# Kernel tuning notes

Measured on AMD Instinct MI355X. Metric: run time of the kernel, lower is better.

## Reference

```python
import jax, jax.numpy as jnp
import numpy as np

# dims (see shape_source)
B, NC, DIM_IN = 4, 4095, 64      # batch, cells, invariant state dim (n-6)
D, H, L, K = 128, 4, 2, 6        # d_model, heads, layers, num_neighbors
DH = D // H                      # dim_head = 32
HR, NRBF = 16, 16                # radial hidden dim (d_model//8), rbf basis
RBF_MAX, RBF_W = 4.0, 0.25


def _ln(x, s, b):
    m = x.mean(-1, keepdims=True)
    v = x.var(-1, keepdims=True)
    return (x - m) / jnp.sqrt(v + 1e-5) * s + b


def setup_inputs() -> dict:
    key = jax.random.key(0)
    ks = jax.random.split(key, 32)
    def nrm(k, shape, scale):
        return jax.random.normal(k, shape, jnp.float32) * scale
    p = {}
    p['X'] = nrm(ks[0], (B, NC, 6 + DIM_IN), 1.0)
    p['W_embed'] = nrm(ks[1], (DIM_IN, D), DIM_IN ** -0.5)
    p['b_embed'] = jnp.zeros((D,), jnp.float32)
    p['Wq'] = nrm(ks[2], (L, D, D), D ** -0.5)
    p['Wk'] = nrm(ks[3], (L, D, D), D ** -0.5)
    p['Wv'] = nrm(ks[4], (L, D, D), D ** -0.5)
    p['Wvv'] = nrm(ks[5], (L, D, D), D ** -0.5)
    p['rw1'] = nrm(ks[6], (L, NRBF, HR), NRBF ** -0.5)
    p['rb1'] = jnp.zeros((L, HR), jnp.float32)
    p['rw2'] = nrm(ks[7], (L, HR, 2 * D), HR ** -0.5)
    p['rb2'] = jnp.zeros((L, 2 * D), jnp.float32)
    p['Wo'] = nrm(ks[8], (L, D, D), D ** -0.5)
    p['Wov'] = nrm(ks[9], (L, D, D), D ** -0.5)
    p['ff_w1'] = nrm(ks[10], (L, D, 2 * D), D ** -0.5)
    p['ff_b1'] = jnp.zeros((L, 2 * D), jnp.float32)
    p['ff_w2'] = nrm(ks[11], (L, 2 * D, D), (2 * D) ** -0.5)
    p['ff_b2'] = jnp.zeros((L, D), jnp.float32)
    p['gate_w'] = nrm(ks[12], (L, D, D), D ** -0.5)
    p['gate_b'] = jnp.zeros((L, D), jnp.float32)
    p['ln1_s'] = jnp.ones((L, D), jnp.float32)
    p['ln1_b'] = jnp.zeros((L, D), jnp.float32)
    p['ln2_s'] = jnp.ones((L, D), jnp.float32)
    p['ln2_b'] = jnp.zeros((L, D), jnp.float32)
    p['W_state'] = nrm(ks[13], (D, DIM_IN), D ** -0.5)
    p['b_state'] = jnp.zeros((DIM_IN,), jnp.float32)
    p['W_force'] = nrm(ks[14], (D, 1), D ** -0.5)
    p['b_force'] = jnp.zeros((1,), jnp.float32)
    return p


def _forward(X, W_embed, b_embed, Wq, Wk, Wv, Wvv, rw1, rb1, rw2, rb2, Wo, Wov,
             ff_w1, ff_b1, ff_w2, ff_b2, gate_w, gate_b,
             ln1_s, ln1_b, ln2_s, ln2_b, W_state, b_state, W_force, b_force):
    N = NC + 1  # one extra zero node prepended, as in the torch wrapper
    pos = jnp.concatenate([jnp.zeros((B, 1, 3), X.dtype), X[:, :, 0:3]], axis=1)       # [B,N,3]
    feats = jnp.concatenate([jnp.zeros((B, 1, DIM_IN), X.dtype), X[:, :, 6:]], axis=1)  # [B,N,dim_in]

    # k-nearest-neighbor graph (indices are non-differentiable constants)
    d2 = jnp.sum((pos[:, :, None, :] - pos[:, None, :, :]) ** 2, axis=-1)  # [B,N,N]
    d2 = d2 + jnp.eye(N, dtype=X.dtype) * 1e9                               # exclude self
    _, idx = jax.lax.top_k(-d2, K)                                           # [B,N,K]

    gat = lambda a: jax.vmap(lambda ai, ii: ai[ii])(a, idx)  # [B,N,...] -> [B,N,K,...]

    rel = gat(pos) - pos[:, :, None, :]                      # [B,N,K,3]
    dist = jnp.sqrt(jnp.sum(rel ** 2, axis=-1) + 1e-8)       # [B,N,K]
    u = rel / dist[..., None]                                # unit vectors (degree-1 SH)
    centers = jnp.linspace(0.0, RBF_MAX, NRBF).astype(X.dtype)
    rbf = jnp.exp(-((dist[..., None] - centers) / RBF_W) ** 2)  # [B,N,K,NRBF]

    x0 = feats @ W_embed + b_embed                           # type-0 (invariant) feats
    x1 = jnp.zeros((B, N, D, 3), X.dtype)                    # type-1 (vector) feats

    for l in range(L):
        h = _ln(x0, ln1_s[l], ln1_b[l])
        q = (h @ Wq[l]).reshape(B, N, H, DH)
        kj = gat(h @ Wk[l]).reshape(B, N, K, H, DH)
        vj = gat(h @ Wv[l])                                   # [B,N,K,D]
        # radial MLP on distances -> invariant edge weights
        rad = jax.nn.silu(rbf @ rw1[l] + rb1[l]) @ rw2[l] + rb2[l]  # [B,N,K,2D]
        rg, rv = rad[..., :D], rad[..., D:]
        bias = rg.reshape(B, N, K, H, DH).mean(-1)            # [B,N,K,H]
        logits = jnp.einsum('bnhd,bnkhd->bnhk', q, kj) / np.float32(np.sqrt(DH))
        logits = logits + bias.transpose(0, 1, 3, 2)
        attn = jax.nn.softmax(logits, axis=-1)                # over K neighbors
        # degree-0 messages
        m0 = (vj * jax.nn.silu(rv)).reshape(B, N, K, H, DH)
        out0 = jnp.einsum('bnhk,bnkhd->bnhd', attn, m0).reshape(B, N, D)
        x0 = x0 + out0 @ Wo[l]
        # degree-1 messages: channel-mixed neighbor vectors + radial-weighted unit dirs
        x1j = gat(x1)                                          # [B,N,K,D,3]
        m1 = jnp.einsum('bnkdc,de->bnkec', x1j, Wvv[l]) + rv[..., None] * u[:, :, :, None, :]
        m1 = m1.reshape(B, N, K, H, DH, 3)
        out1 = jnp.einsum('bnhk,bnkhdc->bnhdc', attn, m1).reshape(B, N, D, 3)
        x1 = x1 + jnp.einsum('bndc,de->bnec', out1, Wov[l])
        # feed-forward on invariants + invariant gating of vectors (equivariant)
        h2 = _ln(x0, ln2_s[l], ln2_b[l])
        x0 = x0 + jax.nn.silu(h2 @ ff_w1[l] + ff_b1[l]) @ ff_w2[l] + ff_b2[l]
        x1 = x1 * jax.nn.sigmoid(h2 @ gate_w[l] + gate_b[l])[..., None]

    y0 = x0[:, 1:]                                            # drop extra node
    y1 = jnp.swapaxes(x1[:, 1:], -1, -2)                      # [B,NC,3,D]
    state_update = y0 @ W_state + b_state                     # [B,NC,dim_in]
    forces = (y1 @ W_force + b_force)[..., 0]                 # [B,NC,3]
    forces = forces - forces.mean(axis=1, keepdims=True)      # remove net force
    return state_update, forces


def reference(X, W_embed, b_embed, Wq, Wk, Wv, Wvv, rw1, rb1, rw2, rb2, Wo, Wov,
              ff_w1, ff_b1, ff_w2, ff_b2, gate_w, gate_b,
              ln1_s, ln1_b, ln2_s, ln2_b, W_state, b_state, W_force, b_force):
    return _forward(X, W_embed, b_embed, Wq, Wk, Wv, Wvv, rw1, rb1, rw2, rb2, Wo, Wov,
                    ff_w1, ff_b1, ff_w2, ff_b2, gate_w, gate_b,
                    ln1_s, ln1_b, ln2_s, ln2_b, W_state, b_state, W_force, b_force)
```

## Files before the change

### kernel.cpp

```cpp
#include <hip/hip_runtime.h>
#include <cstdint>
#include <cstddef>

namespace {

constexpr int B_ = 4, NC_ = 4095, N_ = 4096, DIN_ = 64, D_ = 128, K_ = 6;
constexpr int XROW_ = 6 + DIN_;
constexpr int ROWS_ = B_ * N_;
constexpr int KNQ = 2;
constexpr int KCAP = 32;

typedef unsigned short u16;
typedef unsigned int u32;
typedef unsigned long long u64;
typedef __attribute__((ext_vector_type(8))) short short8;
typedef __attribute__((ext_vector_type(8))) unsigned short ushort8;
typedef __attribute__((ext_vector_type(4))) float f32x4;

__device__ __forceinline__ float sigm(float x) { return 1.f / (1.f + expf(-x)); }
__device__ __forceinline__ float silu(float x) { return x / (1.f + expf(-x)); }
__device__ __forceinline__ u16 f2bf(float x) {
    u32 u = __float_as_uint(x);
    u += 0x7FFFu + ((u >> 16) & 1u);
    return (u16)(u >> 16);
}
__device__ __forceinline__ float bf2f(u16 x) {
    return __uint_as_float(((u32)x) << 16);
}

__global__ void k_prep(const float* __restrict__ X, float4* __restrict__ pos4,
                       u16* __restrict__ featsb)
{
    int g = blockIdx.x * 256 + threadIdx.x;
    if (g >= ROWS_ * 64) return;
    int c = g & 63, row = g >> 6;
    int b = row >> 12, n = row & (N_ - 1);
    const float* xr = X + (size_t)(b * NC_ + n - 1) * XROW_;
    featsb[g] = (n > 0) ? f2bf(xr[6 + c]) : (u16)0;
    if (c == 0) {
        float4 p = {0.f, 0.f, 0.f, 0.f};
        if (n > 0) { p.x = xr[0]; p.y = xr[1]; p.z = xr[2]; }
        pos4[row] = p;
    }
}

__device__ __forceinline__ u64 shflxor64(u64 v, int mask)
{
    int lo = __shfl_xor((int)(u32)(v & 0xffffffffull), mask, 64);
    int hi = __shfl_xor((int)(u32)(v >> 32), mask, 64);
    return ((u64)(u32)hi << 32) | (u32)lo;
}

__device__ __forceinline__ float kth6min(float v)
{
    const float BIG = 3.4e38f;
    float kth = BIG;
    #pragma unroll
    for (int r = 0; r < 6; ++r) {
        float m = v;
        #pragma unroll
        for (int off = 1; off < 64; off <<= 1) m = fminf(m, __shfl_xor(m, off, 64));
        kth = m;
        if (v == m) v = BIG;
    }
    return kth;
}

__device__ __forceinline__ void geom_write(const float4* __restrict__ pb, int q, int j,
                                           size_t e, float* __restrict__ uv,
                                           float* __restrict__ rbfv)
{
    float4 pj = pb[j], pn = pb[q];
    float rx = pj.x - pn.x, ry = pj.y - pn.y, rz = pj.z - pn.z;
    float dist = sqrtf(rx * rx + ry * ry + rz * rz + 1e-8f);
    float inv = 1.f / dist;
    uv[e * 3 + 0] = rx * inv; uv[e * 3 + 1] = ry * inv; uv[e * 3 + 2] = rz * inv;
    #pragma unroll
    for (int r = 0; r < 16; ++r) {
        float t = (dist - (4.0f / 15.0f) * r) * 4.0f;
        rbfv[e * 16 + r] = expf(-t * t);
    }
}

__global__ __launch_bounds__(256) void k_knn(const float4* __restrict__ pos4,
                                             int* __restrict__ idxv,
                                             float* __restrict__ uv,
                                             float* __restrict__ rbfv)
{
    __shared__ u64 sHits[4][KNQ][KCAP];
    __shared__ int sCnt[4][KNQ];
    const int w = threadIdx.x >> 6, lane = threadIdx.x & 63;
    const int wave = (blockIdx.x << 2) | w;
    const int b = wave >> 11;
    const int i0 = (wave & 2047) << 1;
    const float4* pb = pos4 + (size_t)b * N_;
    const float BIG = 3.4e38f;

    if (lane < KNQ) sCnt[w][lane] = 0;
    __syncthreads();

    float4 qv[KNQ];
    #pragma unroll
    for (int qq = 0; qq < KNQ; ++qq) qv[qq] = pb[i0 + qq];

    float dmin[KNQ];
    #pragma unroll
    for (int qq = 0; qq < KNQ; ++qq) dmin[qq] = BIG;
    #pragma unroll 4
    for (int it = 0; it < 64; ++it) {
        int j = lane + (it << 6);
        float4 p = pb[j];
        #pragma unroll
        for (int qq = 0; qq < KNQ; ++qq) {
            float dx = p.x - qv[qq].x, dy = p.y - qv[qq].y, dz = p.z - qv[qq].z;
            float dd = dx * dx + dy * dy + dz * dz;
            if (j != i0 + qq) dmin[qq] = fminf(dmin[qq], dd);
        }
    }
    float T[KNQ];
    #pragma unroll
    for (int qq = 0; qq < KNQ; ++qq) T[qq] = kth6min(dmin[qq]) * 1.000002f;

    #pragma unroll 4
    for (int it = 0; it < 64; ++it) {
        int j = lane + (it << 6);
        float4 p = pb[j];
        #pragma unroll
        for (int qq = 0; qq < KNQ; ++qq) {
            float dx = p.x - qv[qq].x, dy = p.y - qv[qq].y, dz = p.z - qv[qq].z;
            float dd = dx * dx + dy * dy + dz * dz;
            if (dd <= T[qq] && j != i0 + qq) {
                int slot = atomicAdd(&sCnt[w][qq], 1);
                if (slot < KCAP)
                    sHits[w][qq][slot] = ((u64)__float_as_uint(dd) << 32) | (u32)j;
            }
        }
    }
    __syncthreads();

    const int g = lane >> 5, li = lane & 31;
    const int cnt = sCnt[w][g];
    const int q = i0 + g;
    u64 ent = (li < (cnt < KCAP ? cnt : KCAP)) ? sHits[w][g][li] : ~0ull;
    int myj = -1;
    #pragma unroll
    for (int k = 0; k < 6; ++k) {
        u64 m = ent;
        #pragma unroll
        for (int off = 1; off < 32; off <<= 1) {
            u64 o = shflxor64(m, off);
            if (o < m) m = o;
        }
        if (li == k) myj = (int)(u32)(m & 0xffffffffull);
        if (ent == m) ent = ~0ull;
    }
    if (cnt <= KCAP && li < 6) {
        size_t e = (size_t)(b * N_ + q) * 6 + li;
        idxv[e] = myj;
        geom_write(pb, q, myj, e, uv, rbfv);
    }

    u64 ovf = __ballot(li == 0 && cnt > KCAP);
    while (ovf) {
        int gl = __ffsll(ovf) - 1; ovf &= ovf - 1;
        int qq = gl >> 5;
        int qx = i0 + qq;
        float4 qp = pb[qx];
        float Tq = T[0];
        #pragma unroll
        for (int z = 1; z < KNQ; ++z) if (z == qq) Tq = T[z];
        float e0 = BIG, e1 = BIG, e2 = BIG, e3 = BIG, e4 = BIG, e5 = BIG;
        int j0 = 0, j1 = 0, j2 = 0, j3 = 0, j4 = 0, j5 = 0;
        for (int it = 0; it < 64; ++it) {
            int j = lane + (it << 6);
            float4 p = pb[j];
            float dx = p.x - qp.x, dy = p.y - qp.y, dz = p.z - qp.z;
            float dd = dx * dx + dy * dy + dz * dz;
            if (dd <= Tq && j != qx && dd < e5) {
                e5 = dd; j5 = j;
                float td; int tj;
                if (e5 < e4) { td = e4; e4 = e5; e5 = td; tj = j4; j4 = j5; j5 = tj; }
                if (e4 < e3) { td = e3; e3 = e4; e4 = td; tj = j3; j3 = j4; j4 = tj; }
                if (e3 < e2) { td = e2; e2 = e3; e3 = td; tj = j2; j2 = j3; j3 = tj; }
                if (e2 < e1) { td = e1; e1 = e2; e2 = td; tj = j1; j1 = j2; j2 = tj; }
                if (e1 < e0) { td = e0; e0 = e1; e1 = td; tj = j0; j0 = j1; j1 = tj; }
            }
        }
        u64 a0 = ((u64)__float_as_uint(e0) << 32) | (u32)j0;
        u64 a1 = ((u64)__float_as_uint(e1) << 32) | (u32)j1;
        u64 a2 = ((u64)__float_as_uint(e2) << 32) | (u32)j2;
        u64 a3 = ((u64)__float_as_uint(e3) << 32) | (u32)j3;
        u64 a4 = ((u64)__float_as_uint(e4) << 32) | (u32)j4;
        u64 a5 = ((u64)__float_as_uint(e5) << 32) | (u32)j5;
        int fj = -1;
        #pragma unroll
        for (int k = 0; k < 6; ++k) {
            u64 m = a0;
            #pragma unroll
            for (int off = 1; off < 64; off <<= 1) {
                u64 o = shflxor64(m, off);
                if (o < m) m = o;
            }
            if (a0 == m) { a0 = a1; a1 = a2; a2 = a3; a3 = a4; a4 = a5; a5 = ~0ull; }
            if (lane == k) fj = (int)(u32)(m & 0xffffffffull);
        }
        if (lane < 6) {
            size_t e = (size_t)(b * N_ + qx) * 6 + lane;
            idxv[e] = fj;
            geom_write(pb, qx, fj, e, uv, rbfv);
        }
    }
}

__global__ void k_prepw(const float* __restrict__ Wq, const float* __restrict__ Wk,
                        const float* __restrict__ Wv, const float* __restrict__ gw,
                        const float* __restrict__ fw1, const float* __restrict__ gb_,
                        const float* __restrict__ fb1, const float* __restrict__ Wvv,
                        const float* __restrict__ Wov, const float* __restrict__ Wo_,
                        const float* __restrict__ fw2, const float* __restrict__ rw2,
                        const float* __restrict__ rb2, const float* __restrict__ W_embed,
                        const float* __restrict__ rw1,
                        u16* __restrict__ WqkvT, u16* __restrict__ Wc2T,
                        u16* __restrict__ WvvT, u16* __restrict__ WovT,
                        u16* __restrict__ WoT, u16* __restrict__ fw2T,
                        u16* __restrict__ WembT,
                        float* __restrict__ bias2, float* __restrict__ rwg,
                        float* __restrict__ rw1T, float* __restrict__ rw2vT)
{
    const int l = blockIdx.y;
    int g = blockIdx.x * 256 + threadIdx.x;
    const float* Wq_l = Wq + l * 16384;  const float* Wk_l = Wk + l * 16384;
    const float* Wv_l = Wv + l * 16384;  const float* gw_l = gw + l * 16384;
    const float* fw1_l = fw1 + l * 32768; const float* gb_l = gb_ + l * 128;
    const float* fb1_l = fb1 + l * 256;  const float* Wvv_l = Wvv + l * 16384;
    const float* Wov_l = Wov + l * 16384; const float* Wo_ll = Wo_ + l * 16384;
    const float* fw2_l = fw2 + l * 32768; const float* rw2_l = rw2 + l * 4096;
    const float* rb2_l = rb2 + l * 256;  const float* rw1_l = rw1 + l * 256;

    if (g < 49152) {
        int n = g >> 7, k = g & 127;
        const float* src = (n < 128) ? Wq_l : ((n < 256) ? Wk_l : Wv_l);
        WqkvT[l * 49152 + g] = f2bf(src[k * 128 + (n & 127)]); return;
    }
    g -= 49152;
    if (g < 49152) {
        int n = g >> 7, k = g & 127;
        Wc2T[l * 49152 + g] = f2bf((n < 128) ? gw_l[k * 128 + n] : fw1_l[k * 256 + (n - 128)]); return;
    }
    g -= 49152;
    if (g < 16384) { int n = g >> 7, k = g & 127; WvvT[l * 16384 + g] = f2bf(Wvv_l[k * 128 + n]); return; }
    g -= 16384;
    if (g < 16384) { int n = g >> 7, k = g & 127; WovT[l * 16384 + g] = f2bf(Wov_l[k * 128 + n]); return; }
    g -= 16384;
    if (g < 16384) { int n = g >> 7, k = g & 127; WoT[l * 16384 + g] = f2bf(Wo_ll[k * 128 + n]); return; }
    g -= 16384;
    if (g < 32768) { int n = g >> 8, k = g & 255; fw2T[l * 32768 + g] = f2bf(fw2_l[k * 128 + n]); return; }
    g -= 32768;
    if (g < 384) { bias2[l * 384 + g] = (g < 128) ? gb_l[g] : fb1_l[g - 128]; return; }
    g -= 384;
    if (g < 64) {
        int hh = g >> 2, h = g & 3;
        float a = 0.f;
        #pragma unroll
        for (int dh = 0; dh < 32; ++dh) a += rw2_l[hh * 256 + h * 32 + dh];
        rwg[l * 128 + g] = a * (1.f / 32.f); return;
    }
    g -= 64;
    if (g < 4) {
        float a = 0.f;
        #pragma unroll
        for (int dh = 0; dh < 32; ++dh) a += rb2_l[g * 32 + dh];
        rwg[l * 128 + 64 + g] = a * (1.f / 32.f); return;
    }
    g -= 4;
    if (g < 256) {
        int hh = g >> 4, rr = g & 15;
        rw1T[l * 256 + hh * 16 + rr] = rw1_l[rr * 16 + hh]; return;
    }
    g -= 256;
    if (g < 2048) {
        int t = g >> 4, hh = g & 15;
        rw2vT[l * 2048 + t * 16 + hh] = rw2_l[hh * 256 + 128 + t]; return;
    }
    g -= 2048;
    if (g < 8192 && l == 0) {
        int n = g >> 6, k = g & 63;
        WembT[g] = f2bf(W_embed[k * 128 + n]);
    }
}

template<int KD, int BM, int EPI, bool LN, bool X1ACC>
__global__ __launch_bounds__(256) void k_mgemm(
    const u16* __restrict__ A, const u16* __restrict__ WT,
    const float* __restrict__ bias, const float* __restrict__ aux,
    float* __restrict__ C, u16* __restrict__ Cb, int ldc,
    const float* __restrict__ lns, const float* __restrict__ lnb,
    u16* __restrict__ lnout)
{
    constexpr int MI = BM / 16;
    __shared__ u16 sA[BM * 40];
    __shared__ u16 sB[128 * 40];
    const int tid = threadIdx.x;
    const int lane = tid & 63, wn = tid >> 6;
    const int m0 = blockIdx.x * BM, n0 = blockIdx.y * 128;
    f32x4 acc[MI][2] = {};

    for (int k0 = 0; k0 < KD; k0 += 32) {
        __syncthreads();
        if (BM == 64) {
            int row = tid >> 2, gk = tid & 3;
            *(uint4*)&sA[row * 40 + gk * 8] =
                *(const uint4*)&A[(size_t)(m0 + row) * KD + k0 + gk * 8];
        } else {
            if (tid < BM * 4) {
                int row = tid >> 2, gk = tid & 3;
                *(uint4*)&sA[row * 40 + gk * 8] =
                    *(const uint4*)&A[(size_t)(m0 + row) * KD + k0 + gk * 8];
            }
        }
        #pragma unroll
        for (int cc = 0; cc < 2; ++cc) {
            int c = tid * 2 + cc;
            int row = c >> 2, gk = c & 3;
            *(uint4*)&sB[row * 40 + gk * 8] =
                *(const uint4*)&WT[(size_t)(n0 + row) * KD + k0 + gk * 8];
        }
        __syncthreads();
        const int gk = lane >> 4, lr = lane & 15;
        short8 af[MI], bfr[2];
        #pragma unroll
        for (int i = 0; i < MI; ++i)
            af[i] = *(const short8*)&sA[(i * 16 + lr) * 40 + gk * 8];
        #pragma unroll
        for (int i = 0; i < 2; ++i)
            bfr[i] = *(const short8*)&sB[(wn * 32 + i * 16 + lr) * 40 + gk * 8];
        #pragma unroll
        for (int mi = 0; mi < MI; ++mi)
            #pragma unroll
            for (int ni = 0; ni < 2; ++ni)
                acc[mi][ni] = __builtin_amdgcn_mfma_f32_16x16x32_bf16(af[mi], bfr[ni], acc[mi][ni], 0, 0, 0);
    }

    const int lg = lane >> 4;
    const int lc = lane & 15;
    if (LN) {
        __shared__ float sLN[BM][4][2];
        float s1[MI][4], s2[MI][4];
        #pragma unroll
        for (int mi = 0; mi < MI; ++mi) {
            int rbase = m0 + mi * 16 + lg * 4;
            #pragma unroll
            for (int ee = 0; ee < 4; ++ee) { s1[mi][ee] = 0.f; s2[mi][ee] = 0.f; }
            #pragma unroll
            for (int ni = 0; ni < 2; ++ni) {
                int col = wn * 32 + ni * 16 + lc;
                float bc = bias ? bias[col] : 0.f;
                #pragma unroll
                for (int ee = 0; ee < 4; ++ee) {
                    float v = acc[mi][ni][ee] + bc;
                    if (EPI == 1) v += C[(size_t)(rbase + ee) * 128 + col];
                    acc[mi][ni][ee] = v;
                    s1[mi][ee] += v;
                    s2[mi][ee] += v * v;
                }
            }
        }
        #pragma unroll
        for (int mi = 0; mi < MI; ++mi)
            #pragma unroll
            for (int ee = 0; ee < 4; ++ee)
                #pragma unroll
                for (int off = 1; off < 16; off <<= 1) {
                    s1[mi][ee] += __shfl_xor(s1[mi][ee], off, 64);
                    s2[mi][ee] += __shfl_xor(s2[mi][ee], off, 64);
                }
        if (lc == 0) {
            #pragma unroll
            for (int mi = 0; mi < MI; ++mi)
                #pragma unroll
                for (int ee = 0; ee < 4; ++ee) {
                    int r = mi * 16 + lg * 4 + ee;
                    sLN[r][wn][0] = s1[mi][ee];
                    sLN[r][wn][1] = s2[mi][ee];
                }
        }
        __syncthreads();
        #pragma unroll
        for (int mi = 0; mi < MI; ++mi) {
            int rbase = m0 + mi * 16 + lg * 4;
            #pragma unroll
            for (int ee = 0; ee < 4; ++ee) {
                int r = mi * 16 + lg * 4 + ee;
                float sum = sLN[r][0][0] + sLN[r][1][0] + sLN[r][2][0] + sLN[r][3][0];
                float sq  = sLN[r][0][1] + sLN[r][1][1] + sLN[r][2][1] + sLN[r][3][1];
                float mean = sum * (1.f / 128.f);
                float var = sq * (1.f / 128.f) - mean * mean;
                float inv = 1.f / sqrtf(var + 1e-5f);
                #pragma unroll
                for (int ni = 0; ni < 2; ++ni) {
// ... 9 lines not shown
    }

    #pragma unroll
    for (int mi = 0; mi < MI; ++mi) {
        int rbase = m0 + mi * 16 + lg * 4;
        #pragma unroll
        for (int ni = 0; ni < 2; ++ni) {
            int col = n0 + wn * 32 + ni * 16 + lc;
            if (EPI == 0) {
                float bc = bias ? bias[col] : 0.f;
                #pragma unroll
                for (int ee = 0; ee < 4; ++ee)
                    C[(size_t)(rbase + ee) * ldc + col] = acc[mi][ni][ee] + bc;
            } else if (EPI == 1) {
                float bc = bias ? bias[col] : 0.f;
                #pragma unroll
                for (int ee = 0; ee < 4; ++ee) {
                    size_t o = (size_t)(rbase + ee) * ldc + col;
                    C[o] += acc[mi][ni][ee] + bc;
                }
            } else if (EPI == 2) {
                float bc = bias[col];
                if (n0 == 0) {
                    #pragma unroll
                    for (int ee = 0; ee < 4; ++ee)
                        C[(size_t)(rbase + ee) * 128 + col] = sigm(acc[mi][ni][ee] + bc);
                } else {
                    int c2 = col - 128;
                    #pragma unroll
                    for (int ee = 0; ee < 4; ++ee)
                        Cb[(size_t)(rbase + ee) * 256 + c2] = f2bf(silu(acc[mi][ni][ee] + bc));
                }
            } else if (EPI == 4) {
                float bc = bias ? bias[col] : 0.f;
                #pragma unroll
                for (int ee = 0; ee < 4; ++ee)
                    Cb[(size_t)(rbase + ee) * ldc + col] = f2bf(acc[mi][ni][ee] + bc);
            } else {
                #pragma unroll
                for (int ee = 0; ee < 4; ++ee) {
                    int m = rbase + ee;
                    size_t o = (size_t)m * 128 + col;
                    float v = acc[mi][ni][ee];
                    if (X1ACC) v += C[o];
                    v *= aux[(size_t)(m / 3) * 128 + col];
                    C[o] = v;
                    Cb[o] = f2bf(v);
                }
            }
        }
    }
}

template<int KD>
__global__ __launch_bounds__(256) void k_tgemm(
    const float* __restrict__ A, const float* __restrict__ W, const float* __restrict__ bias,
    float* __restrict__ C, int ldw, int ldc)
{
    __shared__ __align__(16) float As[32 * 132];
    __shared__ __align__(16) float Ws[32 * 68];
    const int tid = threadIdx.x;
    const int tx = tid & 15, ty = tid >> 4;
    const int m0 = blockIdx.x * 128, n0 = blockIdx.y * 64;
    float acc[8][4] = {};
    for (int k0 = 0; k0 < KD; k0 += 32) {
        __syncthreads();
        #pragma unroll
        for (int r = 0; r < 4; ++r) {
            int id = tid + r * 256;
            int row = id >> 3, kq = id & 7;
            float4 a4 = *(const float4*)&A[(size_t)(m0 + row) * KD + k0 + kq * 4];
            As[(kq * 4 + 0) * 132 + row] = a4.x;
            As[(kq * 4 + 1) * 132 + row] = a4.y;
            As[(kq * 4 + 2) * 132 + row] = a4.z;
            As[(kq * 4 + 3) * 132 + row] = a4.w;
        }
        #pragma unroll
        for (int r = 0; r < 2; ++r) {
            int id = tid + r * 256;
            int kr = id >> 4, cq = id & 15;
            *(float4*)&Ws[kr * 68 + cq * 4] =
                *(const float4*)&W[(size_t)(k0 + kr) * ldw + n0 + cq * 4];
        }
        __syncthreads();
        #pragma unroll 8
        for (int k = 0; k < 32; ++k) {
            float4 aA = *(const float4*)&As[k * 132 + ty * 8];
            float4 aB = *(const float4*)&As[k * 132 + ty * 8 + 4];
            float4 w4 = *(const float4*)&Ws[k * 68 + tx * 4];
            float av[8] = {aA.x, aA.y, aA.z, aA.w, aB.x, aB.y, aB.z, aB.w};
            float wv[4] = {w4.x, w4.y, w4.z, w4.w};
            #pragma unroll
            for (int r = 0; r < 8; ++r)
                #pragma unroll
                for (int j = 0; j < 4; ++j)
                    acc[r][j] += av[r] * wv[j];
        }
    }
    float bv[4];
    #pragma unroll
    for (int j = 0; j < 4; ++j) bv[j] = bias[n0 + tx * 4 + j];
    #pragma unroll
    for (int r = 0; r < 8; ++r) {
        int m = m0 + ty * 8 + r;
        int n = m & (N_ - 1), bb2 = m >> 12;
        if (n == 0) continue;
        float* dst = C + ((size_t)(bb2 * NC_ + n - 1)) * ldc + n0 + tx * 4;
        float4 res = {acc[r][0] + bv[0], acc[r][1] + bv[1], acc[r][2] + bv[2], acc[r][3] + bv[3]};
        *(float4*)dst = res;
    }
}

template<bool HASY1>
__global__ __launch_bounds__(256) void k_attn(
    const u16* __restrict__ qkvb, const int* __restrict__ idxv,
    const float* __restrict__ rbfv, const float* __restrict__ uv,
    const u16* __restrict__ y1b,
    const float* __restrict__ rw1T, const float* __restrict__ rb1,
    const float* __restrict__ rw2vT, const float* __restrict__ rwg,
    const float* __restrict__ rb2,
    u16* __restrict__ o0b, u16* __restrict__ o1b)
{
    const int wid = threadIdx.x >> 6, lane = threadIdx.x & 63;
    const int row = blockIdx.x * 4 + wid;
    const int b = row >> 12;
    const int ch0 = lane * 2;
    const int h = lane >> 4;

    __shared__ float sHid[4][6][16];
    __shared__ float sU[4][6][3];

    int jl = 0;
    if (lane < 6) jl = idxv[row * 6 + lane];
    int jj[6];
    #pragma unroll
    for (int k = 0; k < 6; ++k) jj[k] = __shfl(jl, k, 64);

    if (lane < 18) sU[wid][lane / 3][lane % 3] = uv[(size_t)row * 18 + lane];

    {
        int idx = lane;
        #pragma unroll
        for (int rep = 0; rep < 2; ++rep) {
            if (idx < 96) {
                int k = idx >> 4, hh = idx & 15;
                float a = rb1[hh];
                const float* rb = rbfv + (size_t)(row * 6 + k) * 16;
                const float* wr = rw1T + hh * 16;
                #pragma unroll
                for (int rr = 0; rr < 16; ++rr) a += rb[rr] * wr[rr];
                sHid[wid][k][hh] = silu(a);
            }
            idx += 64;
        }
    }
    __builtin_amdgcn_wave_barrier();
    __threadfence_block();
    __builtin_amdgcn_wave_barrier();

    u32 qp = *(const u32*)&qkvb[(size_t)row * 384 + ch0];
    float q0 = bf2f((u16)qp), q1 = bf2f((u16)(qp >> 16));

// ... 29 lines not shown
    for (int k = 0; k < 6; ++k) a[k] *= inv;

    float rwc0[16], rwc1[16];
    {
        const float4* wp = (const float4*)(rw2vT + ch0 * 16);
        #pragma unroll
        for (int i = 0; i < 4; ++i) {
            float4 v0 = wp[i], v1 = wp[i + 4];
            rwc0[i * 4 + 0] = v0.x; rwc0[i * 4 + 1] = v0.y; rwc0[i * 4 + 2] = v0.z; rwc0[i * 4 + 3] = v0.w;
            rwc1[i * 4 + 0] = v1.x; rwc1[i * 4 + 1] = v1.y; rwc1[i * 4 + 2] = v1.z; rwc1[i * 4 + 3] = v1.w;
        }
    }
    float rb20 = rb2[128 + ch0], rb21 = rb2[128 + ch0 + 1];
    float rvk0[6], rvk1[6];
    #pragma unroll
    for (int k = 0; k < 6; ++k) {
        float a0 = rb20, a1 = rb21;
        #pragma unroll
        for (int hh = 0; hh < 16; ++hh) {
            float hv = sHid[wid][k][hh];
            a0 += hv * rwc0[hh];
            a1 += hv * rwc1[hh];
        }
        rvk0[k] = a0; rvk1[k] = a1;
    }

    float o00 = 0.f, o01 = 0.f;
    #pragma unroll
    for (int k = 0; k < 6; ++k) {
        u32 vp = *(const u32*)&qkvb[(size_t)(b * N_ + jj[k]) * 384 + 256 + ch0];
        o00 += a[k] * bf2f((u16)vp) * silu(rvk0[k]);
        o01 += a[k] * bf2f((u16)(vp >> 16)) * silu(rvk1[k]);
    }
    *(u32*)&o0b[(size_t)row * 128 + ch0] = (u32)f2bf(o00) | ((u32)f2bf(o01) << 16);

    #pragma unroll
    for (int c = 0; c < 3; ++c) {
        float s0 = 0.f, s1 = 0.f;
        #pragma unroll
        for (int k = 0; k < 6; ++k) {
            float b0 = 0.f, b1 = 0.f;
            if (HASY1) {
                u32 yp = *(const u32*)&y1b[((size_t)(b * N_ + jj[k]) * 3 + c) * 128 + ch0];
                b0 = bf2f((u16)yp); b1 = bf2f((u16)(yp >> 16));
            }
            float uk = sU[wid][k][c];
            s0 += a[k] * (b0 + rvk0[k] * uk);
            s1 += a[k] * (b1 + rvk1[k] * uk);
        }
        *(u32*)&o1b[((size_t)row * 3 + c) * 128 + ch0] = (u32)f2bf(s0) | ((u32)f2bf(s1) << 16);
    }
}

__global__ void k_force1(const float* __restrict__ x1, const float* __restrict__ W,
                         const float* __restrict__ bias, float* __restrict__ frc)
{
    int g = blockIdx.x * 256 + threadIdx.x;
    if (g >= B_ * NC_ * 3) return;
    int c = g % 3, rr = g / 3;
    int b = rr / NC_, n = rr - b * NC_;
    const float* xr = x1 + (size_t)(b * N_ + n + 1) * 384 + c * 128;
    float a = bias[0];
    for (int d = 0; d < 128; ++d) a += xr[d] * W[d];
    frc[g] = a;
}

__global__ __launch_bounds__(256) void k_fsum(const float* __restrict__ frc, float* __restrict__ fsum)
{
    int b = blockIdx.x / 3, c = blockIdx.x % 3;
    __shared__ float red[256];
    float a = 0.f;
    for (int n = threadIdx.x; n < NC_; n += 256) a += frc[(b * NC_ + n) * 3 + c];
    red[threadIdx.x] = a; __syncthreads();
    for (int st = 128; st > 0; st >>= 1) { if (threadIdx.x < st) red[threadIdx.x] += red[threadIdx.x + st]; __syncthreads(); }
    if (threadIdx.x == 0) fsum[blockIdx.x] = red[0] / (float)NC_;
}

__global__ void k_force2(const float* __restrict__ frc, const float* __restrict__ fsum,
                         float* __restrict__ out)
{
    int g = blockIdx.x * 256 + threadIdx.x;
    if (g >= B_ * NC_ * 3) return;
    int c = g % 3;
    int b = g / (NC_ * 3);
    out[g] = frc[g] - fsum[b * 3 + c];
}

}

extern "C" void kernel_launch(void* const* d_in, const int* in_sizes, int n_in,
                              void* d_out, int out_size, void* d_ws, size_t ws_size,
                              hipStream_t stream)
{
    const float* X       = (const float*)d_in[0];
    const float* W_embed = (const float*)d_in[1];
    const float* b_embed = (const float*)d_in[2];
    const float* Wq      = (const float*)d_in[3];
    const float* Wk      = (const float*)d_in[4];
    const float* Wv      = (const float*)d_in[5];
    const float* Wvv     = (const float*)d_in[6];
    const float* rw1     = (const float*)d_in[7];
    const float* rb1     = (const float*)d_in[8];
    const float* rw2     = (const float*)d_in[9];
    const float* rb2     = (const float*)d_in[10];
    const float* Wo      = (const float*)d_in[11];
    const float* Wov     = (const float*)d_in[12];
    const float* ff_w1   = (const float*)d_in[13];
    const float* ff_b1   = (const float*)d_in[14];
    const float* ff_w2   = (const float*)d_in[15];
    const float* ff_b2   = (const float*)d_in[16];
    const float* gate_w  = (const float*)d_in[17];
    const float* gate_b  = (const float*)d_in[18];
    const float* ln1_s   = (const float*)d_in[19];
    const float* ln1_b   = (const float*)d_in[20];
    const float* ln2_s   = (const float*)d_in[21];
    const float* ln2_b   = (const float*)d_in[22];
    const float* W_state = (const float*)d_in[23];
    const float* b_state = (const float*)d_in[24];
    const float* W_force = (const float*)d_in[25];
    const float* b_force = (const float*)d_in[26];
    (void)in_sizes; (void)n_in; (void)out_size; (void)ws_size;

    float* out = (float*)d_out;
    float* w = (float*)d_ws;

    float4* pos4  = (float4*)w;
    int*    idxv  = (int*)(w + 65536);
    float*  uv    = w + 163840;
    float*  rbfv  = w + 458752;
    u16*    featsb= (u16*)(w + 2031616);
    float*  x0    = w + 2555904;
    u16*    hbb   = (u16*)(w + 4653056);
    u16*    qkvbb = (u16*)(w + 5701632);
    float*  gb    = w + 11993088;
    u16*    o0b   = (u16*)(w + 14090240);
    u16*    o1b   = (u16*)(w + 15138816);
    float*  x1    = w + 18284544;
    u16*    x1b   = (u16*)(w + 24576000);
    u16*    t1b   = (u16*)(w + 27721728);
    u16*    y1b   = t1b;
    u16*    WqkvT = (u16*)(w + 34013184);
    u16*    Wc2T  = (u16*)(w + 34062336);
    u16*    WvvT  = (u16*)(w + 34111488);
    u16*    WovT  = (u16*)(w + 34127872);
    u16*    WoT   = (u16*)(w + 34144256);
    u16*    fw2T  = (u16*)(w + 34160640);
    u16*    WembT = (u16*)(w + 34193408);
    float*  bias2 = w + 34197504;
    float*  rwg   = w + 34198272;
    float*  rw1T  = w + 34198528;
    float*  rw2vT = w + 34199040;
    float*  frc   = (float*)featsb;
    float*  fsum  = ((float*)featsb) + 49152;

    k_prepw<<<dim3(747, 2), 256, 0, stream>>>(Wq, Wk, Wv, gate_w, ff_w1, gate_b, ff_b1,
                                              Wvv, Wov, Wo, ff_w2, rw2, rb2, W_embed, rw1,
                                              WqkvT, Wc2T, WvvT, WovT, WoT, fw2T, WembT,
                                              bias2, rwg, rw1T, rw2vT);
    k_prep<<<(ROWS_ * 64 + 255) / 256, 256, 0, stream>>>(X, pos4, featsb);
    k_knn<<<ROWS_ / 8, 256, 0, stream>>>(pos4, idxv, uv, rbfv);
    k_mgemm<64, 32, 0, true, true><<<dim3(512, 1), 256, 0, stream>>>(
        featsb, WembT, b_embed, nullptr, x0, nullptr, 128, ln1_s, ln1_b, hbb);

    for (int l = 0; l < 2; ++l) {
        const float* rb1_l = rb1 + l * 16;
        const float* rb2_l = rb2 + l * 256;
        const float* fb2_l = ff_b2 + l * 128;

        k_mgemm<128, 64, 4, false, true><<<dim3(256, 3), 256, 0, stream>>>(
            hbb, WqkvT + l * 49152, nullptr, nullptr, nullptr, qkvbb, 384, nullptr, nullptr, nullptr);
        if (l > 0)
            k_mgemm<128, 64, 4, false, true><<<dim3(768, 1), 256, 0, stream>>>(
                x1b, WvvT + l * 16384, nullptr, nullptr, nullptr, y1b, 128, nullptr, nullptr, nullptr);
        if (l == 0)
            k_attn<false><<<ROWS_ / 4, 256, 0, stream>>>(qkvbb, idxv, rbfv, uv, nullptr,
                rw1T + l * 256, rb1_l, rw2vT + l * 2048, rwg + l * 128, rb2_l, o0b, o1b);
        else
            k_attn<true><<<ROWS_ / 4, 256, 0, stream>>>(qkvbb, idxv, rbfv, uv, y1b,
                rw1T + l * 256, rb1_l, rw2vT + l * 2048, rwg + l * 128, rb2_l, o0b, o1b);
        k_mgemm<128, 32, 1, true, true><<<dim3(512, 1), 256, 0, stream>>>(
            o0b, WoT + l * 16384, nullptr, nullptr, x0, nullptr, 128,
            ln2_s + l * 128, ln2_b + l * 128, hbb);
        k_mgemm<128, 64, 2, false, true><<<dim3(256, 3), 256, 0, stream>>>(
            hbb, Wc2T + l * 49152, bias2 + l * 384, nullptr, gb, t1b, 128, nullptr, nullptr, nullptr);
        if (l == 0)
            k_mgemm<128, 64, 3, false, false><<<dim3(768, 1), 256, 0, stream>>>(
                o1b, WovT + l * 16384, nullptr, gb, x1, x1b, 128, nullptr, nullptr, nullptr);
        else
            k_mgemm<128, 64, 3, false, true><<<dim3(768, 1), 256, 0, stream>>>(
                o1b, WovT + l * 16384, nullptr, gb, x1, x1b, 128, nullptr, nullptr, nullptr);
        if (l == 0)
            k_mgemm<256, 32, 1, true, true><<<dim3(512, 1), 256, 0, stream>>>(
                t1b, fw2T + l * 32768, fb2_l, nullptr, x0, nullptr, 128,
                ln1_s + 128, ln1_b + 128, hbb);
        else
            k_mgemm<256, 32, 1, false, true><<<dim3(512, 1), 256, 0, stream>>>(
                t1b, fw2T + l * 32768, fb2_l, nullptr, x0, nullptr, 128, nullptr, nullptr, nullptr);
    }

    k_tgemm<128><<<dim3(128, 1), 256, 0, stream>>>(x0, W_state, b_state, out, 64, 64);
    k_force1<<<(B_ * NC_ * 3 + 255) / 256, 256, 0, stream>>>(x1, W_force, b_force, frc);
    k_fsum<<<12, 256, 0, stream>>>(frc, fsum);
    k_force2<<<(B_ * NC_ * 3 + 255) / 256, 256, 0, stream>>>(frc, fsum, out + (size_t)B_ * NC_ * DIN_);
}
```

Measured before the change: 315.5 us.

## Merge independent kernels into combined launches to cut launch count

Combines weight and input prep into one launch and pairs independent GEMMs (QKV with Wvv, Wov with FF2) into dual-body kernels dispatched by block index. The output-state GEMM and the force projection share a single head kernel. The KNN threshold pass now takes the 7th-smallest distance including self instead of excluding self with a per-element check. The goal is fewer launches and better occupancy, at the cost of shared-memory sizing fixed to the larger variant and odd dead arithmetic in the force loop.

```diff
diff --git a/kernel.cpp b/kernel.cpp
--- a/kernel.cpp
+++ b/kernel.cpp
@@ -14,7 +14,6 @@
 typedef unsigned int u32;
 typedef unsigned long long u64;
 typedef __attribute__((ext_vector_type(8))) short short8;
-typedef __attribute__((ext_vector_type(8))) unsigned short ushort8;
 typedef __attribute__((ext_vector_type(4))) float f32x4;
 
 __device__ __forceinline__ float sigm(float x) { return 1.f / (1.f + expf(-x)); }
@@ -28,10 +27,9 @@
     return __uint_as_float(((u32)x) << 16);
 }
 
-__global__ void k_prep(const float* __restrict__ X, float4* __restrict__ pos4,
-                       u16* __restrict__ featsb)
-{
-    int g = blockIdx.x * 256 + threadIdx.x;
+__device__ __forceinline__ void prep_body(const float* __restrict__ X, float4* __restrict__ pos4,
+                                          u16* __restrict__ featsb, int g)
+{
     if (g >= ROWS_ * 64) return;
     int c = g & 63, row = g >> 6;
     int b = row >> 12, n = row & (N_ - 1);
@@ -44,6 +42,95 @@
     }
 }
 
+__device__ __forceinline__ void prepw_body(int l, int g,
+    const float* Wq, const float* Wk, const float* Wv, const float* gw,
+    const float* fw1, const float* gb_, const float* fb1, const float* Wvv,
+    const float* Wov, const float* Wo_, const float* fw2, const float* rw2,
+    const float* rb2, const float* W_embed, const float* rw1,
+    u16* WqkvT, u16* Wc2T, u16* WvvT, u16* WovT, u16* WoT, u16* fw2T, u16* WembT,
+    float* bias2, float* rwg, float* rw1T, float* rw2vT)
+{
+    const float* Wq_l = Wq + l * 16384;  const float* Wk_l = Wk + l * 16384;
+    const float* Wv_l = Wv + l * 16384;  const float* gw_l = gw + l * 16384;
+    const float* fw1_l = fw1 + l * 32768; const float* gb_l = gb_ + l * 128;
+    const float* fb1_l = fb1 + l * 256;  const float* Wvv_l = Wvv + l * 16384;
+    const float* Wov_l = Wov + l * 16384; const float* Wo_ll = Wo_ + l * 16384;
+    const float* fw2_l = fw2 + l * 32768; const float* rw2_l = rw2 + l * 4096;
+    const float* rb2_l = rb2 + l * 256;  const float* rw1_l = rw1 + l * 256;
+
+    if (g < 49152) {
+        int n = g >> 7, k = g & 127;
+        const float* src = (n < 128) ? Wq_l : ((n < 256) ? Wk_l : Wv_l);
+        WqkvT[l * 49152 + g] = f2bf(src[k * 128 + (n & 127)]); return;
+    }
+    g -= 49152;
+    if (g < 49152) {
+        int n = g >> 7, k = g & 127;
+        Wc2T[l * 49152 + g] = f2bf((n < 128) ? gw_l[k * 128 + n] : fw1_l[k * 256 + (n - 128)]); return;
+    }
+    g -= 49152;
+    if (g < 16384) { int n = g >> 7, k = g & 127; WvvT[l * 16384 + g] = f2bf(Wvv_l[k * 128 + n]); return; }
+    g -= 16384;
+    if (g < 16384) { int n = g >> 7, k = g & 127; WovT[l * 16384 + g] = f2bf(Wov_l[k * 128 + n]); return; }
+    g -= 16384;
+    if (g < 16384) { int n = g >> 7, k = g & 127; WoT[l * 16384 + g] = f2bf(Wo_ll[k * 128 + n]); return; }
+    g -= 16384;
+    if (g < 32768) { int n = g >> 8, k = g & 255; fw2T[l * 32768 + g] = f2bf(fw2_l[k * 128 + n]); return; }
+    g -= 32768;
+    if (g < 384) { bias2[l * 384 + g] = (g < 128) ? gb_l[g] : fb1_l[g - 128]; return; }
+    g -= 384;
+    if (g < 64) {
+        int hh = g >> 2, h = g & 3;
+        float a = 0.f;
+        #pragma unroll
+        for (int dh = 0; dh < 32; ++dh) a += rw2_l[hh * 256 + h * 32 + dh];
+        rwg[l * 128 + g] = a * (1.f / 32.f); return;
+    }
+    g -= 64;
+    if (g < 4) {
+        float a = 0.f;
+        #pragma unroll
+        for (int dh = 0; dh < 32; ++dh) a += rb2_l[g * 32 + dh];
+        rwg[l * 128 + 64 + g] = a * (1.f / 32.f); return;
+    }
+    g -= 4;
+    if (g < 256) {
+        int hh = g >> 4, rr = g & 15;
+        rw1T[l * 256 + hh * 16 + rr] = rw1_l[rr * 16 + hh]; return;
+    }
+    g -= 256;
+    if (g < 2048) {
+        int t = g >> 4, hh = g & 15;
+        rw2vT[l * 2048 + t * 16 + hh] = rw2_l[hh * 256 + 128 + t]; return;
+    }
+    g -= 2048;
+    if (g < 8192 && l == 0) {
+        int n = g >> 6, k = g & 63;
+        WembT[g] = f2bf(W_embed[k * 128 + n]);
+    }
+}
+
+__global__ void k_prepall(const float* __restrict__ X, float4* __restrict__ pos4,
+                          u16* __restrict__ featsb,
+                          const float* Wq, const float* Wk, const float* Wv, const float* gw,
+                          const float* fw1, const float* gb_, const float* fb1, const float* Wvv,
+                          const float* Wov, const float* Wo_, const float* fw2, const float* rw2,
+                          const float* rb2, const float* W_embed, const float* rw1,
+                          u16* WqkvT, u16* Wc2T, u16* WvvT, u16* WovT, u16* WoT, u16* fw2T,
+                          u16* WembT, float* bias2, float* rwg, float* rw1T, float* rw2vT)
+{
+    int id = blockIdx.x;
+    if (id < 4096) {
+        prep_body(X, pos4, featsb, id * 256 + threadIdx.x);
+    } else {
+        int id2 = id - 4096;
+        int l = id2 / 747, gx = id2 % 747;
+        prepw_body(l, gx * 256 + threadIdx.x, Wq, Wk, Wv, gw, fw1, gb_, fb1, Wvv, Wov, Wo_,
+                   fw2, rw2, rb2, W_embed, rw1, WqkvT, Wc2T, WvvT, WovT, WoT, fw2T, WembT,
+                   bias2, rwg, rw1T, rw2vT);
+    }
+}
+
 __device__ __forceinline__ u64 shflxor64(u64 v, int mask)
 {
     int lo = __shfl_xor((int)(u32)(v & 0xffffffffull), mask, 64);
@@ -51,12 +138,12 @@
     return ((u64)(u32)hi << 32) | (u32)lo;
 }
 
-__device__ __forceinline__ float kth6min(float v)
+__device__ __forceinline__ float kth7min(float v)
 {
     const float BIG = 3.4e38f;
     float kth = BIG;
     #pragma unroll
-    for (int r = 0; r < 6; ++r) {
+    for (int r = 0; r < 7; ++r) {
         float m = v;
         #pragma unroll
         for (int off = 1; off < 64; off <<= 1) m = fminf(m, __shfl_xor(m, off, 64));
@@ -114,12 +201,12 @@
         for (int qq = 0; qq < KNQ; ++qq) {
             float dx = p.x - qv[qq].x, dy = p.y - qv[qq].y, dz = p.z - qv[qq].z;
             float dd = dx * dx + dy * dy + dz * dz;
-            if (j != i0 + qq) dmin[qq] = fminf(dmin[qq], dd);
+            dmin[qq] = fminf(dmin[qq], dd);
         }
     }
     float T[KNQ];
     #pragma unroll
-    for (int qq = 0; qq < KNQ; ++qq) T[qq] = kth6min(dmin[qq]) * 1.000002f;
+    for (int qq = 0; qq < KNQ; ++qq) T[qq] = kth7min(dmin[qq]) * 1.000002f;
 
     #pragma unroll 4
     for (int it = 0; it < 64; ++it) {
@@ -212,97 +299,20 @@
     }
 }
 
-__global__ void k_prepw(const float* __restrict__ Wq, const float* __restrict__ Wk,
-                        const float* __restrict__ Wv, const float* __restrict__ gw,
-                        const float* __restrict__ fw1, const float* __restrict__ gb_,
-                        const float* __restrict__ fb1, const float* __restrict__ Wvv,
-                        const float* __restrict__ Wov, const float* __restrict__ Wo_,
-                        const float* __restrict__ fw2, const float* __restrict__ rw2,
-                        const float* __restrict__ rb2, const float* __restrict__ W_embed,
-                        const float* __restrict__ rw1,
-                        u16* __restrict__ WqkvT, u16* __restrict__ Wc2T,
-                        u16* __restrict__ WvvT, u16* __restrict__ WovT,
-                        u16* __restrict__ WoT, u16* __restrict__ fw2T,
-                        u16* __restrict__ WembT,
-                        float* __restrict__ bias2, float* __restrict__ rwg,
-                        float* __restrict__ rw1T, float* __restrict__ rw2vT)
-{
-    const int l = blockIdx.y;
-    int g = blockIdx.x * 256 + threadIdx.x;
-    const float* Wq_l = Wq + l * 16384;  const float* Wk_l = Wk + l * 16384;
-    const float* Wv_l = Wv + l * 16384;  const float* gw_l = gw + l * 16384;
-    const float* fw1_l = fw1 + l * 32768; const float* gb_l = gb_ + l * 128;
-    const float* fb1_l = fb1 + l * 256;  const float* Wvv_l = Wvv + l * 16384;
-    const float* Wov_l = Wov + l * 16384; const float* Wo_ll = Wo_ + l * 16384;
-    const float* fw2_l = fw2 + l * 32768; const float* rw2_l = rw2 + l * 4096;
-    const float* rb2_l = rb2 + l * 256;  const float* rw1_l = rw1 + l * 256;
-
-    if (g < 49152) {
-        int n = g >> 7, k = g & 127;
-        const float* src = (n < 128) ? Wq_l : ((n < 256) ? Wk_l : Wv_l);
-        WqkvT[l * 49152 + g] = f2bf(src[k * 128 + (n & 127)]); return;
-    }
-    g -= 49152;
-    if (g < 49152) {
-        int n = g >> 7, k = g & 127;
-        Wc2T[l * 49152 + g] = f2bf((n < 128) ? gw_l[k * 128 + n] : fw1_l[k * 256 + (n - 128)]); return;
-    }
-    g -= 49152;
-    if (g < 16384) { int n = g >> 7, k = g & 127; WvvT[l * 16384 + g] = f2bf(Wvv_l[k * 128 + n]); return; }
-    g -= 16384;
-    if (g < 16384) { int n = g >> 7, k = g & 127; WovT[l * 16384 + g] = f2bf(Wov_l[k * 128 + n]); return; }
-    g -= 16384;
-    if (g < 16384) { int n = g >> 7, k = g & 127; WoT[l * 16384 + g] = f2bf(Wo_ll[k * 128 + n]); return; }
-    g -= 16384;
-    if (g < 32768) { int n = g >> 8, k = g & 255; fw2T[l * 32768 + g] = f2bf(fw2_l[k * 128 + n]); return; }
-    g -= 32768;
-    if (g < 384) { bias2[l * 384 + g] = (g < 128) ? gb_l[g] : fb1_l[g - 128]; return; }
-    g -= 384;
-    if (g < 64) {
-        int hh = g >> 2, h = g & 3;
-        float a = 0.f;
-        #pragma unroll
-        for (int dh = 0; dh < 32; ++dh) a += rw2_l[hh * 256 + h * 32 + dh];
-        rwg[l * 128 + g] = a * (1.f / 32.f); return;
-    }
-    g -= 64;
-    if (g < 4) {
-        float a = 0.f;
-        #pragma unroll
-        for (int dh = 0; dh < 32; ++dh) a += rb2_l[g * 32 + dh];
-        rwg[l * 128 + 64 + g] = a * (1.f / 32.f); return;
-    }
-    g -= 4;
-    if (g < 256) {
-        int hh = g >> 4, rr = g & 15;
-        rw1T[l * 256 + hh * 16 + rr] = rw1_l[rr * 16 + hh]; return;
-    }
-    g -= 256;
-    if (g < 2048) {
-        int t = g >> 4, hh = g & 15;
-        rw2vT[l * 2048 + t * 16 + hh] = rw2_l[hh * 256 + 128 + t]; return;
-    }
-    g -= 2048;
-    if (g < 8192 && l == 0) {
-        int n = g >> 6, k = g & 63;
-        WembT[g] = f2bf(W_embed[k * 128 + n]);
-    }
-}
-
 template<int KD, int BM, int EPI, bool LN, bool X1ACC>
-__global__ __launch_bounds__(256) void k_mgemm(
+__device__ __forceinline__ void mgemm_body(
     const u16* __restrict__ A, const u16* __restrict__ WT,
     const float* __restrict__ bias, const float* __restrict__ aux,
     float* __restrict__ C, u16* __restrict__ Cb, int ldc,
     const float* __restrict__ lns, const float* __restrict__ lnb,
-    u16* __restrict__ lnout)
+    u16* __restrict__ lnout,
+    int bx, int by, u16* sA, u16* sB, float* sLNraw)
 {
     constexpr int MI = BM / 16;
-    __shared__ u16 sA[BM * 40];
-    __shared__ u16 sB[128 * 40];
+    float (*sLN)[4][2] = (float(*)[4][2])sLNraw;
     const int tid = threadIdx.x;
     const int lane = tid & 63, wn = tid >> 6;
-    const int m0 = blockIdx.x * BM, n0 = blockIdx.y * 128;
+    const int m0 = bx * BM, n0 = by * 128;
     f32x4 acc[MI][2] = {};
 
     for (int k0 = 0; k0 < KD; k0 += 32) {
@@ -344,7 +354,6 @@
     const int lg = lane >> 4;
     const int lc = lane & 15;
     if (LN) {
-        __shared__ float sLN[BM][4][2];
         float s1[MI][4], s2[MI][4];
         #pragma unroll
         for (int mi = 0; mi < MI; ++mi) {
@@ -460,62 +469,41 @@
     }
 }
 
-template<int KD>
-__global__ __launch_bounds__(256) void k_tgemm(
-    const float* __restrict__ A, const float* __restrict__ W, const float* __restrict__ bias,
-    float* __restrict__ C, int ldw, int ldc)
-{
-    __shared__ __align__(16) float As[32 * 132];
-    __shared__ __align__(16) float Ws[32 * 68];
-    const int tid = threadIdx.x;
-    const int tx = tid & 15, ty = tid >> 4;
-    const int m0 = blockIdx.x * 128, n0 = blockIdx.y * 64;
-    float acc[8][4] = {};
-    for (int k0 = 0; k0 < KD; k0 += 32) {
-        __syncthreads();
-        #pragma unroll
-        for (int r = 0; r < 4; ++r) {
-            int id = tid + r * 256;
-            int row = id >> 3, kq = id & 7;
-            float4 a4 = *(const float4*)&A[(size_t)(m0 + row) * KD + k0 + kq * 4];
-            As[(kq * 4 + 0) * 132 + row] = a4.x;
-            As[(kq * 4 + 1) * 132 + row] = a4.y;
-            As[(kq * 4 + 2) * 132 + row] = a4.z;
-            As[(kq * 4 + 3) * 132 + row] = a4.w;
-        }
-        #pragma unroll
-        for (int r = 0; r < 2; ++r) {
-            int id = tid + r * 256;
-            int kr = id >> 4, cq = id & 15;
-            *(float4*)&Ws[kr * 68 + cq * 4] =
-                *(const float4*)&W[(size_t)(k0 + kr) * ldw + n0 + cq * 4];
-        }
-        __syncthreads();
-        #pragma unroll 8
-        for (int k = 0; k < 32; ++k) {
-            float4 aA = *(const float4*)&As[k * 132 + ty * 8];
-            float4 aB = *(const float4*)&As[k * 132 + ty * 8 + 4];
-            float4 w4 = *(const float4*)&Ws[k * 68 + tx * 4];
-            float av[8] = {aA.x, aA.y, aA.z, aA.w, aB.x, aB.y, aB.z, aB.w};
-            float wv[4] = {w4.x, w4.y, w4.z, w4.w};
-            #pragma unroll
-            for (int r = 0; r < 8; ++r)
-                #pragma unroll
-                for (int j = 0; j < 4; ++j)
-                    acc[r][j] += av[r] * wv[j];
-        }
-    }
-    float bv[4];
-    #pragma unroll
-    for (int j = 0; j < 4; ++j) bv[j] = bias[n0 + tx * 4 + j];
-    #pragma unroll
-    for (int r = 0; r < 8; ++r) {
-        int m = m0 + ty * 8 + r;
-        int n = m & (N_ - 1), bb2 = m >> 12;
-        if (n == 0) continue;
-        float* dst = C + ((size_t)(bb2 * NC_ + n - 1)) * ldc + n0 + tx * 4;
-        float4 res = {acc[r][0] + bv[0], acc[r][1] + bv[1], acc[r][2] + bv[2], acc[r][3] + bv[3]};
-        *(float4*)dst = res;
+template<int KD, int BM, int EPI, bool LN, bool X1ACC>
+__global__ __launch_bounds__(256) void k_mgemm(
+    const u16* __restrict__ A, const u16* __restrict__ WT,
+    const float* __restrict__ bias, const float* __restrict__ aux,
+    float* __restrict__ C, u16* __restrict__ Cb, int ldc,
+    const float* __restrict__ lns, const float* __restrict__ lnb,
+    u16* __restrict__ lnout)
+{
+    __shared__ u16 sA[64 * 40];
+    __shared__ u16 sB[128 * 40];
+    __shared__ float sLN[64 * 4 * 2];
+    mgemm_body<KD, BM, EPI, LN, X1ACC>(A, WT, bias, aux, C, Cb, ldc, lns, lnb, lnout,
+                                       blockIdx.x, blockIdx.y, sA, sB, sLN);
+}
+
+template<int KD0, int BM0, int EPI0, bool LN0, bool XA0,
+         int KD1, int BM1, int EPI1, bool LN1v, bool XA1>
+__global__ __launch_bounds__(256) void k_mgemm_dual(
+    const u16* A0, const u16* WT0, const float* b0, const float* aux0,
+    float* C0, u16* Cb0, int ldc0, const float* lns0, const float* lnb0, u16* ln0,
+    int nx0, int nxdiv0,
+    const u16* A1, const u16* WT1, const float* b1, const float* aux1,
+    float* C1, u16* Cb1, int ldc1, const float* lns1, const float* lnb1, u16* ln1)
+{
+    __shared__ u16 sA[64 * 40];
+    __shared__ u16 sB[128 * 40];
+    __shared__ float sLN[64 * 4 * 2];
+    int id = blockIdx.x;
+    if (id < nx0) {
+        mgemm_body<KD0, BM0, EPI0, LN0, XA0>(A0, WT0, b0, aux0, C0, Cb0, ldc0, lns0, lnb0, ln0,
+                                             id % nxdiv0, id / nxdiv0, sA, sB, sLN);
+    } else {
+        id -= nx0;
+        mgemm_body<KD1, BM1, EPI1, LN1v, XA1>(A1, WT1, b1, aux1, C1, Cb1, ldc1, lns1, lnb1, ln1,
+                                              id, 0, sA, sB, sLN);
     }
 }
 
@@ -651,17 +639,75 @@
     }
 }
 
-__global__ void k_force1(const float* __restrict__ x1, const float* __restrict__ W,
-                         const float* __restrict__ bias, float* __restrict__ frc)
-{
-    int g = blockIdx.x * 256 + threadIdx.x;
-    if (g >= B_ * NC_ * 3) return;
-    int c = g % 3, rr = g / 3;
-    int b = rr / NC_, n = rr - b * NC_;
-    const float* xr = x1 + (size_t)(b * N_ + n + 1) * 384 + c * 128;
-    float a = bias[0];
-    for (int d = 0; d < 128; ++d) a += xr[d] * W[d];
-    frc[g] = a;
+__global__ __launch_bounds__(256) void k_head(
+    const float* __restrict__ x0, const float* __restrict__ W_state,
+    const float* __restrict__ b_state, float* __restrict__ out,
+    const float* __restrict__ x1, const float* __restrict__ W_force,
+    const float* __restrict__ b_force, float* __restrict__ frc)
+{
+    __shared__ __align__(16) float As[32 * 132];
+    __shared__ __align__(16) float Ws[32 * 68];
+    const int tid = threadIdx.x;
+    if (blockIdx.x < 128) {
+        const int tx = tid & 15, ty = tid >> 4;
+        const int m0 = blockIdx.x * 128, n0 = 0;
+        float acc[8][4] = {};
+        for (int k0 = 0; k0 < 128; k0 += 32) {
+            __syncthreads();
+            #pragma unroll
+            for (int r = 0; r < 4; ++r) {
+                int id = tid + r * 256;
+                int row = id >> 3, kq = id & 7;
+                float4 a4 = *(const float4*)&x0[(size_t)(m0 + row) * 128 + k0 + kq * 4];
+                As[(kq * 4 + 0) * 132 + row] = a4.x;
+                As[(kq * 4 + 1) * 132 + row] = a4.y;
+                As[(kq * 4 + 2) * 132 + row] = a4.z;
+                As[(kq * 4 + 3) * 132 + row] = a4.w;
+            }
+            #pragma unroll
+            for (int r = 0; r < 2; ++r) {
+                int id = tid + r * 256;
+                int kr = id >> 4, cq = id & 15;
+                *(float4*)&Ws[kr * 68 + cq * 4] =
+                    *(const float4*)&W_state[(size_t)(k0 + kr) * 64 + n0 + cq * 4];
+            }
+            __syncthreads();
+            #pragma unroll 8
+            for (int k = 0; k < 32; ++k) {
+                float4 aA = *(const float4*)&As[k * 132 + ty * 8];
+                float4 aB = *(const float4*)&As[k * 132 + ty * 8 + 4];
+                float4 w4 = *(const float4*)&Ws[k * 68 + tx * 4];
+                float av[8] = {aA.x, aA.y, aA.z, aA.w, aB.x, aB.y, aB.z, aB.w};
+                float wv[4] = {w4.x, w4.y, w4.z, w4.w};
+                #pragma unroll
+                for (int r = 0; r < 8; ++r)
+                    #pragma unroll
+                    for (int j = 0; j < 4; ++j)
+                        acc[r][j] += av[r] * wv[j];
+            }
+        }
+        float bv[4];
+        #pragma unroll
+        for (int j = 0; j < 4; ++j) bv[j] = b_state[n0 + tx * 4 + j];
+        #pragma unroll
+        for (int r = 0; r < 8; ++r) {
+            int m = m0 + ty * 8 + r;
+            int n = m & (N_ - 1), bb2 = m >> 12;
+            if (n == 0) continue;
+            float* dst = out + ((size_t)(bb2 * NC_ + n - 1)) * 64 + n0 + tx * 4;
+            float4 res = {acc[r][0] + bv[0], acc[r][1] + bv[1], acc[r][2] + bv[2], acc[r][3] + bv[3]};
+            *(float4*)dst = res;
+        }
+    } else {
+        int g = (blockIdx.x - 128) * 256 + tid;
+        if (g >= B_ * NC_ * 3) return;
+        int c = g % 3, rr = g / 3;
+        int b = rr / NC_, n = rr - b * NC_;
+        const float* xr = x1 + (size_t)(b * N_ + n + 1) * 384 + c * 128;
+        float a = b_force[0];
+        for (int d = 0; d < 128; ++d) a += xr[d * 3 - d * 3 + d] * 0.f + xr[d] * W_force[d];
+        frc[g] = a;
+    }
 }
 
 __global__ __launch_bounds__(256) void k_fsum(const float* __restrict__ frc, float* __restrict__ fsum)
@@ -752,11 +798,11 @@
     float*  frc   = (float*)featsb;
     float*  fsum  = ((float*)featsb) + 49152;
 
-    k_prepw<<<dim3(747, 2), 256, 0, stream>>>(Wq, Wk, Wv, gate_w, ff_w1, gate_b, ff_b1,
-                                              Wvv, Wov, Wo, ff_w2, rw2, rb2, W_embed, rw1,
-                                              WqkvT, Wc2T, WvvT, WovT, WoT, fw2T, WembT,
-                                              bias2, rwg, rw1T, rw2vT);
-    k_prep<<<(ROWS_ * 64 + 255) / 256, 256, 0, stream>>>(X, pos4, featsb);
+    k_prepall<<<5590, 256, 0, stream>>>(X, pos4, featsb,
+                                        Wq, Wk, Wv, gate_w, ff_w1, gate_b, ff_b1,
+                                        Wvv, Wov, Wo, ff_w2, rw2, rb2, W_embed, rw1,
+                                        WqkvT, Wc2T, WvvT, WovT, WoT, fw2T, WembT,
+                                        bias2, rwg, rw1T, rw2vT);
     k_knn<<<ROWS_ / 8, 256, 0, stream>>>(pos4, idxv, uv, rbfv);
     k_mgemm<64, 32, 0, true, true><<<dim3(512, 1), 256, 0, stream>>>(
         featsb, WembT, b_embed, nullptr, x0, nullptr, 128, ln1_s, ln1_b, hbb);
@@ -766,11 +812,14 @@
         const float* rb2_l = rb2 + l * 256;
         const float* fb2_l = ff_b2 + l * 128;
 
-        k_mgemm<128, 64, 4, false, true><<<dim3(256, 3), 256, 0, stream>>>(
-            hbb, WqkvT + l * 49152, nullptr, nullptr, nullptr, qkvbb, 384, nullptr, nullptr, nullptr);
-        if (l > 0)
-            k_mgemm<128, 64, 4, false, true><<<dim3(768, 1), 256, 0, stream>>>(
-                x1b, WvvT + l * 16384, nullptr, nullptr, nullptr, y1b, 128, nullptr, nullptr, nullptr);
+        if (l == 0)
+            k_mgemm<128, 64, 4, false, true><<<dim3(256, 3), 256, 0, stream>>>(
+                hbb, WqkvT, nullptr, nullptr, nullptr, qkvbb, 384, nullptr, nullptr, nullptr);
+        else
+            k_mgemm_dual<128, 64, 4, false, true, 128, 64, 4, false, true><<<1536, 256, 0, stream>>>(
+                hbb, WqkvT + 49152, nullptr, nullptr, nullptr, qkvbb, 384, nullptr, nullptr, nullptr,
+                768, 256,
+                x1b, WvvT + 16384, nullptr, nullptr, nullptr, y1b, 128, nullptr, nullptr, nullptr);
         if (l == 0)
             k_attn<false><<<ROWS_ / 4, 256, 0, stream>>>(qkvbb, idxv, rbfv, uv, nullptr,
                 rw1T + l * 256, rb1_l, rw2vT + l * 2048, rwg + l * 128, rb2_l, o0b, o1b);
@@ -783,22 +832,18 @@
         k_mgemm<128, 64, 2, false, true><<<dim3(256, 3), 256, 0, stream>>>(
             hbb, Wc2T + l * 49152, bias2 + l * 384, nullptr, gb, t1b, 128, nullptr, nullptr, nullptr);
         if (l == 0)
-            k_mgemm<128, 64, 3, false, false><<<dim3(768, 1), 256, 0, stream>>>(
-                o1b, WovT + l * 16384, nullptr, gb, x1, x1b, 128, nullptr, nullptr, nullptr);
+            k_mgemm_dual<128, 64, 3, false, false, 256, 32, 1, true, true><<<1280, 256, 0, stream>>>(
+                o1b, WovT, nullptr, gb, x1, x1b, 128, nullptr, nullptr, nullptr,
+                768, 768,
+                t1b, fw2T, fb2_l, nullptr, x0, nullptr, 128, ln1_s + 128, ln1_b + 128, hbb);
         else
-            k_mgemm<128, 64, 3, false, true><<<dim3(768, 1), 256, 0, stream>>>(
-                o1b, WovT + l * 16384, nullptr, gb, x1, x1b, 128, nullptr, nullptr, nullptr);
-        if (l == 0)
-            k_mgemm<256, 32, 1, true, true><<<dim3(512, 1), 256, 0, stream>>>(
-                t1b, fw2T + l * 32768, fb2_l, nullptr, x0, nullptr, 128,
-                ln1_s + 128, ln1_b + 128, hbb);
-        else
-            k_mgemm<256, 32, 1, false, true><<<dim3(512, 1), 256, 0, stream>>>(
-                t1b, fw2T + l * 32768, fb2_l, nullptr, x0, nullptr, 128, nullptr, nullptr, nullptr);
-    }
-
-    k_tgemm<128><<<dim3(128, 1), 256, 0, stream>>>(x0, W_state, b_state, out, 64, 64);
-    k_force1<<<(B_ * NC_ * 3 + 255) / 256, 256, 0, stream>>>(x1, W_force, b_force, frc);
+            k_mgemm_dual<128, 64, 3, false, true, 256, 32, 1, false, true><<<1280, 256, 0, stream>>>(
+                o1b, WovT + 16384, nullptr, gb, x1, x1b, 128, nullptr, nullptr, nullptr,
+                768, 768,
+                t1b, fw2T + 32768, fb2_l, nullptr, x0, nullptr, 128, nullptr, nullptr, nullptr);
+    }
+
+    k_head<<<320, 256, 0, stream>>>(x0, W_state, b_state, out, x1, W_force, b_force, frc);
     k_fsum<<<12, 256, 0, stream>>>(frc, fsum);
     k_force2<<<(B_ * NC_ * 3 + 255) / 256, 256, 0, stream>>>(frc, fsum, out + (size_t)B_ * NC_ * DIN_);
 }
```

Measured after the change: 290.7 us. -7.9%, faster.
